# Optimization experiments

Measured on AMD Instinct MI355X. Metric: run time of the kernel, lower is better.

Reference implementation:

```python
import jax, jax.numpy as jnp
import numpy as np

N = 50000
E = 800000
NUM_GRAPHS = 64
D_IN = 261
D_SAGE = 64
D_LIN = 32
N_SAGE_REST = 6
N_LIN_REST = 3
EPS = 1e-5


def _layernorm(x, g, b):
    mu = jnp.mean(x, axis=-1, keepdims=True)
    var = jnp.mean((x - mu) ** 2, axis=-1, keepdims=True)
    return (x - mu) * jax.lax.rsqrt(var + EPS) * g + b


def _sage_block(x, Wl, bl, Wr, g, b, src, dst, inv_deg, residual):
    # mean aggregation of neighbor (source) features onto targets
    msum = jax.ops.segment_sum(x[src], dst, num_segments=N)  # [N, d]
    mean = msum * inv_deg  # [N, d]
    f = mean @ Wl + bl + x @ Wr  # lin_l(aggr) + lin_r(x); lin_r has no bias
    f = jax.nn.gelu(f, approximate=False)
    f = _layernorm(f, g, b)
    if residual:
        f = f + x
    return f


def _lin_block(x, W, b, g, beta, residual):
    f = jax.nn.gelu(x @ W + b, approximate=False)
    f = _layernorm(f, g, beta)
    if residual:
        f = f + x
    return f


def setup_inputs() -> dict:
    key = jax.random.key(0)
    ks = jax.random.split(key, 24)
    x = jax.random.normal(ks[0], (N, D_IN), dtype=jnp.float32)
    edge_index = jax.random.randint(ks[1], (2, E), 0, N, dtype=jnp.int64)
    batch = jnp.sort(jax.random.randint(ks[2], (N,), 0, NUM_GRAPHS, dtype=jnp.int64))

    def glorot(k, shape):
        fan_in = shape[0]
        return jax.random.normal(k, shape, dtype=jnp.float32) / np.sqrt(fan_in)

    inp = {
        "x": x, "edge_index": edge_index, "batch": batch,
        # first SAGE block (261 -> 64, no residual)
        "Wl0": glorot(ks[3], (D_IN, D_SAGE)), "bl0": jnp.zeros((D_SAGE,), jnp.float32),
        "Wr0": glorot(ks[4], (D_IN, D_SAGE)),
        "g0": jnp.ones((D_SAGE,), jnp.float32), "beta0": jnp.zeros((D_SAGE,), jnp.float32),
        # 6 residual SAGE blocks (64 -> 64), stacked
        "Wl": glorot(ks[5], (N_SAGE_REST, D_SAGE, D_SAGE)),
        "bl": jnp.zeros((N_SAGE_REST, D_SAGE), jnp.float32),
        "Wr": glorot(ks[6], (N_SAGE_REST, D_SAGE, D_SAGE)),
        "g": jnp.ones((N_SAGE_REST, D_SAGE), jnp.float32),
        "beta": jnp.zeros((N_SAGE_REST, D_SAGE), jnp.float32),
        # MLP: first LinearBlock 64 -> 32 (no residual)
        "M0": glorot(ks[7], (D_SAGE, D_LIN)), "mb0": jnp.zeros((D_LIN,), jnp.float32),
        "mg0": jnp.ones((D_LIN,), jnp.float32), "mbeta0": jnp.zeros((D_LIN,), jnp.float32),
        # 3 residual LinearBlocks 32 -> 32, stacked
        "M": glorot(ks[8], (N_LIN_REST, D_LIN, D_LIN)),
        "mb": jnp.zeros((N_LIN_REST, D_LIN), jnp.float32),
        "mg": jnp.ones((N_LIN_REST, D_LIN), jnp.float32),
        "mbeta": jnp.zeros((N_LIN_REST, D_LIN), jnp.float32),
        # final Linear 32 -> 1
        "Wf": glorot(ks[9], (D_LIN, 1)), "bf": jnp.zeros((1,), jnp.float32),
    }
    return inp


def reference(x, edge_index, batch, Wl0, bl0, Wr0, g0, beta0, Wl, bl, Wr, g, beta,
              M0, mb0, mg0, mbeta0, M, mb, mg, mbeta, Wf, bf):
    src, dst = edge_index[0], edge_index[1]
    deg = jax.ops.segment_sum(jnp.ones((E,), x.dtype), dst, num_segments=N)
    inv_deg = (1.0 / jnp.maximum(deg, 1.0))[:, None]  # [N,1]

    h = _sage_block(x, Wl0, bl0, Wr0, g0, beta0, src, dst, inv_deg, residual=False)
    for i in range(N_SAGE_REST):
        h = _sage_block(h, Wl[i], bl[i], Wr[i], g[i], beta[i], src, dst, inv_deg, residual=True)

    pooled = jax.ops.segment_sum(h, batch, num_segments=NUM_GRAPHS)  # [G, 64]

    m = _lin_block(pooled, M0, mb0, mg0, mbeta0, residual=False)
    for i in range(N_LIN_REST):
        m = _lin_block(m, M[i], mb[i], mg[i], mbeta[i], residual=True)
    return m @ Wf + bf  # [G, 1]
```

## Files before the change

### kernel.cpp

```cpp
#include <hip/hip_runtime.h>
#include <hip/hip_bf16.h>
#include <math.h>

#define N_NODES 50000
#define N_EDGES 800000
#define NUM_GRAPHS 64
#define NPAD 50048
#define KPAD0 288
#define PSPLIT 16
#define MAXDEG 64

#define GEMM0_GRID (NPAD / 64)
#define SCAT_GRID  ((N_EDGES + 255) / 256)
#define ZERO_GRID  ((N_NODES + 255) / 256)
#define PREPW_TOT  (128 * KPAD0 + 6 * 128 * 64)
#define PREPW_GRID ((PREPW_TOT + 255) / 256)

typedef __attribute__((ext_vector_type(8))) short short8;
typedef __attribute__((ext_vector_type(4))) float f32x4;

__device__ __forceinline__ float gelu_f(float v) {
    return 0.5f * v * (1.0f + erff(v * 0.70710678118654752440f));
}

__device__ __forceinline__ float half_sum32(float v) {
    v += __shfl_xor(v, 1); v += __shfl_xor(v, 2); v += __shfl_xor(v, 4);
    v += __shfl_xor(v, 8); v += __shfl_xor(v, 16);
    return v;
}

__device__ __forceinline__ float group_sum8(float v) {
    v += __shfl_xor(v, 1); v += __shfl_xor(v, 2); v += __shfl_xor(v, 4);
    return v;
}

__device__ __forceinline__ unsigned short f2bf(float f) {
    unsigned int u = __float_as_uint(f);
    unsigned int r = (u + 0x7fffu + ((u >> 16) & 1u)) >> 16;
    return (unsigned short)r;
}

__device__ __forceinline__ float bf_lo(unsigned int u) {
    return __uint_as_float(u << 16);
}
__device__ __forceinline__ float bf_hi(unsigned int u) {
    return __uint_as_float(u & 0xffff0000u);
}


__global__ void k_prep(int* __restrict__ deg,
                       const float* __restrict__ Wl0, const float* __restrict__ Wr0,
                       const float* __restrict__ Wl, const float* __restrict__ Wr,
                       unsigned short* __restrict__ Bt0, unsigned short* __restrict__ BtR) {
    const int blk = blockIdx.x, tid = threadIdx.x;
    if (blk < ZERO_GRID) {
        int i = blk * 256 + tid;
        if (i < N_NODES) deg[i] = 0;
        return;
    }
    int idx = (blk - ZERO_GRID) * 256 + tid;
    const int n0 = 128 * KPAD0;
    if (idx < n0) {
        int j = idx / KPAD0, k = idx - j * KPAD0;
        float v = 0.0f;
        if (k < 261) v = (j < 64) ? Wl0[k * 64 + j] : Wr0[k * 64 + (j - 64)];
        Bt0[idx] = f2bf(v);
    } else if (idx < PREPW_TOT) {
        int r = idx - n0;
        int l = r >> 13;
        int rr = r & 8191;
        int j = rr >> 6, k = rr & 63;
        float v = (j < 64) ? Wl[l * 4096 + k * 64 + j] : Wr[l * 4096 + k * 64 + (j - 64)];
        BtR[r] = f2bf(v);
    }
}


__global__ __launch_bounds__(256) void k_front(
        const float* __restrict__ X, const unsigned short* __restrict__ Bt0,
        unsigned short* __restrict__ U, float* __restrict__ V,
        const int* __restrict__ src, const int* __restrict__ dst,
        int* __restrict__ deg, unsigned short* __restrict__ col64) {
    __shared__ __align__(16) unsigned short sA[64 * 32];
    __shared__ __align__(16) unsigned short sB[128 * 32];
    const int blk = blockIdx.x;
    const int tid = threadIdx.x;

    if (blk < GEMM0_GRID) {
        const int lane = tid & 63, wid = tid >> 6;
        const int l16 = lane & 15, quad = lane >> 4;
        const int m0 = blk * 64;
        f32x4 acc[8];
        #pragma unroll
        for (int j = 0; j < 8; ++j) { acc[j][0] = 0.f; acc[j][1] = 0.f; acc[j][2] = 0.f; acc[j][3] = 0.f; }
        const int arow = tid >> 2, apart = (tid & 3) << 3;
        const int node = m0 + arow;
        const int rowok = (node < N_NODES);
        for (int kc = 0; kc < KPAD0; kc += 32) {
            if (kc) __syncthreads();
            short8 av;
            #pragma unroll
            for (int j = 0; j < 8; ++j) {
                int kk = kc + apart + j;
                float val = (rowok && kk < 261) ? X[(size_t)node * 261 + kk] : 0.0f;
                av[j] = (short)f2bf(val);
            }
            *(short8*)&sA[arow * 32 + apart] = av;
            #pragma unroll
            for (int q = 0; q < 2; ++q) {
                int flat = q * 256 + tid;
                int br = flat >> 2, bp = (flat & 3) << 3;
                *(int4*)&sB[br * 32 + bp] = *(const int4*)&Bt0[(size_t)br * KPAD0 + kc + bp];
            }
            __syncthreads();
            short8 af = *(const short8*)&sA[(wid * 16 + l16) * 32 + quad * 8];
            #pragma unroll
            for (int j = 0; j < 8; ++j) {
                short8 bf = *(const short8*)&sB[(j * 16 + l16) * 32 + quad * 8];
                acc[j] = __builtin_amdgcn_mfma_f32_16x16x32_bf16(af, bf, acc[j], 0, 0, 0);
            }
        }
        const int rbase = m0 + wid * 16 + quad * 4;
        #pragma unroll
        for (int j = 0; j < 4; ++j)
            #pragma unroll
            for (int r = 0; r < 4; ++r)
                U[(size_t)(rbase + r) * 64 + j * 16 + l16] = f2bf(acc[j][r]);
        #pragma unroll
        for (int j = 4; j < 8; ++j)
            #pragma unroll
            for (int r = 0; r < 4; ++r)
                V[(size_t)(rbase + r) * 64 + (j - 4) * 16 + l16] = acc[j][r];
    } else {
        int i = (blk - GEMM0_GRID) * 256 + tid;
        if (i < N_EDGES) {
            int d = dst[i];
            int pos = atomicAdd(&deg[d], 1);
            if (pos < MAXDEG) col64[(d << 6) + pos] = (unsigned short)src[i];
        }
    }
}


__global__ __launch_bounds__(256) void k_layer(
        const unsigned short* __restrict__ U_in, const float* __restrict__ V_in,
        unsigned short* __restrict__ h,
        float* __restrict__ hf_out,
        const int* __restrict__ deg, const unsigned short* __restrict__ col64,
        const float* __restrict__ bias, const float* __restrict__ gam,
        const float* __restrict__ bet,
        const unsigned short* __restrict__ Bt_next,
        unsigned short* __restrict__ U_out, float* __restrict__ V_out,
        int residual, int have_gemm) {
    __shared__ __align__(16) unsigned short sA[2 * 64 * 32];
    __shared__ __align__(16) unsigned short sB[128 * 32];
    const int tid = threadIdx.x;
    const int lane = tid & 63, wid = tid >> 6;
    const int sub = lane >> 3, hl = lane & 7;
    const int base = lane & 56;
    const int m0 = blockIdx.x * 64;
    const uint4* __restrict__ Up = (const uint4*)U_in;

    #pragma unroll
    for (int rep = 0; rep < 2; ++rep) {
        const int nl = rep * 32 + wid * 8 + sub;
        const int node = m0 + nl;
        const bool valid = (node < N_NODES);
        const int nd = valid ? node : 0;
        const int dg = valid ? deg[nd] : 0;
        const int cnt = min(dg, MAXDEG);
        uint4 cv = make_uint4(0u, 0u, 0u, 0u);
        if (valid) cv = *(const uint4*)&col64[((size_t)nd << 6) + hl * 8];
        float s0 = 0.f, s1 = 0.f, s2 = 0.f, s3 = 0.f, s4 = 0.f, s5 = 0.f, s6 = 0.f, s7 = 0.f;
        for (int b = 0; b * 8 < cnt; b += 2) {
            #pragma unroll
            for (int hh = 0; hh < 2; ++hh) {
                const int sl = base + b + hh;
                unsigned int p0 = (unsigned int)__shfl((int)cv.x, sl);
                unsigned int p1 = (unsigned int)__shfl((int)cv.y, sl);
                unsigned int p2 = (unsigned int)__shfl((int)cv.z, sl);
                unsigned int p3 = (unsigned int)__shfl((int)cv.w, sl);
                const int eb = (b + hh) * 8;
                int c[8];
                c[0] = (int)(p0 & 0xffffu); c[1] = (int)(p0 >> 16);
                c[2] = (int)(p1 & 0xffffu); c[3] = (int)(p1 >> 16);
                c[4] = (int)(p2 & 0xffffu); c[5] = (int)(p2 >> 16);
                c[6] = (int)(p3 & 0xffffu); c[7] = (int)(p3 >> 16);
                #pragma unroll
                for (int i = 0; i < 8; ++i) {
                    uint4 u = (eb + i < cnt) ? Up[(size_t)c[i] * 8 + hl] : make_uint4(0u, 0u, 0u, 0u);
                    s0 += bf_lo(u.x); s1 += bf_hi(u.x);
                    s2 += bf_lo(u.y); s3 += bf_hi(u.y);
                    s4 += bf_lo(u.z); s5 += bf_hi(u.z);
                    s6 += bf_lo(u.w); s7 += bf_hi(u.w);
                }
            }
        }
        const float id = 1.0f / fmaxf((float)dg, 1.0f);
        const float4 b0 = *(const float4*)&bias[8 * hl];
        const float4 b1 = *(const float4*)&bias[8 * hl + 4];
        float4 v0 = make_float4(0.f, 0.f, 0.f, 0.f), v1 = v0;
        if (valid) {
            v0 = *(const float4*)&V_in[(size_t)nd * 64 + 8 * hl];
            v1 = *(const float4*)&V_in[(size_t)nd * 64 + 8 * hl + 4];
        }
        float f0 = gelu_f(s0 * id + b0.x + v0.x);
        float f1 = gelu_f(s1 * id + b0.y + v0.y);
        float f2 = gelu_f(s2 * id + b0.z + v0.z);
        float f3 = gelu_f(s3 * id + b0.w + v0.w);
        float f4 = gelu_f(s4 * id + b1.x + v1.x);
        float f5 = gelu_f(s5 * id + b1.y + v1.y);
        float f6 = gelu_f(s6 * id + b1.z + v1.z);
        float f7 = gelu_f(s7 * id + b1.w + v1.w);
        float mu = group_sum8(((f0 + f1) + (f2 + f3)) + ((f4 + f5) + (f6 + f7))) * 0.015625f;
        float d0 = f0 - mu, d1 = f1 - mu, d2 = f2 - mu, d3 = f3 - mu;
        float d4 = f4 - mu, d5 = f5 - mu, d6 = f6 - mu, d7 = f7 - mu;
        float var = group_sum8(((d0 * d0 + d1 * d1) + (d2 * d2 + d3 * d3)) +
                               ((d4 * d4 + d5 * d5) + (d6 * d6 + d7 * d7))) * 0.015625f;
        float rs = rsqrtf(var + 1e-5f);
        const float4 g0v = *(const float4*)&gam[8 * hl];
        const float4 g1v = *(const float4*)&gam[8 * hl + 4];
        const float4 e0v = *(const float4*)&bet[8 * hl];
        const float4 e1v = *(const float4*)&bet[8 * hl + 4];
        f0 = d0 * rs * g0v.x + e0v.x;
        f1 = d1 * rs * g0v.y + e0v.y;
        f2 = d2 * rs * g0v.z + e0v.z;
        f3 = d3 * rs * g0v.w + e0v.w;
        f4 = d4 * rs * g1v.x + e1v.x;
        f5 = d5 * rs * g1v.y + e1v.y;
        f6 = d6 * rs * g1v.z + e1v.z;
        f7 = d7 * rs * g1v.w + e1v.w;
        if (residual && valid) {
            uint4 hu = ((const uint4*)h)[(size_t)nd * 8 + hl];
            f0 += bf_lo(hu.x); f1 += bf_hi(hu.x);
            f2 += bf_lo(hu.y); f3 += bf_hi(hu.y);
            f4 += bf_lo(hu.z); f5 += bf_hi(hu.z);
            f6 += bf_lo(hu.w); f7 += bf_hi(hu.w);
        }
        uint4 outw;
        outw.x = (unsigned int)f2bf(f0) | ((unsigned int)f2bf(f1) << 16);
        outw.y = (unsigned int)f2bf(f2) | ((unsigned int)f2bf(f3) << 16);
        outw.z = (unsigned int)f2bf(f4) | ((unsigned int)f2bf(f5) << 16);
        outw.w = (unsigned int)f2bf(f6) | ((unsigned int)f2bf(f7) << 16);
        if (valid) {
            ((uint4*)h)[(size_t)nd * 8 + hl] = outw;
            if (hf_out) {
                *(float4*)&hf_out[(size_t)nd * 64 + 8 * hl] = make_float4(f0, f1, f2, f3);
                *(float4*)&hf_out[(size_t)nd * 64 + 8 * hl + 4] = make_float4(f4, f5, f6, f7);
            }
        }
        *(uint4*)&sA[(((hl >> 2) * 64 + nl) << 5) + (hl & 3) * 8] = outw;
    }
    if (!have_gemm) return;
    __syncthreads();

    const int l16 = lane & 15, quad = lane >> 4;
    f32x4 acc[8];
    #pragma unroll
    for (int j = 0; j < 8; ++j) { acc[j][0] = 0.f; acc[j][1] = 0.f; acc[j][2] = 0.f; acc[j][3] = 0.f; }
    for (int kc = 0; kc < 64; kc += 32) {
        if (kc) __syncthreads();
        #pragma unroll
        for (int q = 0; q < 2; ++q) {
            int flat = q * 256 + tid;
            int br = flat >> 2, bp = (flat & 3) << 3;
            *(int4*)&sB[br * 32 + bp] = *(const int4*)&Bt_next[(size_t)br * 64 + kc + bp];
        }
        __syncthreads();
        short8 af = *(const short8*)&sA[(((kc >> 5) * 64 + wid * 16 + l16) << 5) + quad * 8];
        #pragma unroll
        for (int j = 0; j < 8; ++j) {
            short8 bf = *(const short8*)&sB[(j * 16 + l16) * 32 + quad * 8];
            acc[j] = __builtin_amdgcn_mfma_f32_16x16x32_bf16(af, bf, acc[j], 0, 0, 0);
        }
    }
    const int rbase = m0 + wid * 16 + quad * 4;
    #pragma unroll
    for (int j = 0; j < 4; ++j)
        #pragma unroll
        for (int r = 0; r < 4; ++r)
            U_out[(size_t)(rbase + r) * 64 + j * 16 + l16] = f2bf(acc[j][r]);
    #pragma unroll
    for (int j = 4; j < 8; ++j)
        #pragma unroll
        for (int r = 0; r < 4; ++r)
            V_out[(size_t)(rbase + r) * 64 + (j - 4) * 16 + l16] = acc[j][r];
}


__global__ __launch_bounds__(256) void k_pool1(const float* __restrict__ h, const int* __restrict__ batch,
                                               float* __restrict__ partial, int n) {
    __shared__ float sred[4][64];
    const int g = blockIdx.x / PSPLIT;
    const int s = blockIdx.x - g * PSPLIT;
    const int lane = threadIdx.x & 63, wid = threadIdx.x >> 6;
    int lo = 0, hi = n;
    while (lo < hi) { int mid = (lo + hi) >> 1; if (batch[mid] < g) lo = mid + 1; else hi = mid; }
    const int start = lo;
    lo = 0; hi = n;
    while (lo < hi) { int mid = (lo + hi) >> 1; if (batch[mid] < g + 1) lo = mid + 1; else hi = mid; }
    const int end = lo;
    const int len = end - start;
    const int chunk = (len + PSPLIT - 1) / PSPLIT;
    const int a = start + s * chunk;
    const int b = min(a + chunk, end);
    float sum = 0.0f;
    for (int node = a + wid; node < b; node += 4) sum += h[(size_t)node * 64 + lane];
    sred[wid][lane] = sum;
    __syncthreads();
    if (wid == 0)
        partial[(size_t)blockIdx.x * 64 + lane] = sred[0][lane] + sred[1][lane] + sred[2][lane] + sred[3][lane];
}


__global__ __launch_bounds__(1024) void k_head(const float* __restrict__ partial,
                                               const float* __restrict__ M0, const float* __restrict__ mb0,
                                               const float* __restrict__ mg0, const float* __restrict__ mbeta0,
                                               const float* __restrict__ M, const float* __restrict__ mb,
                                               const float* __restrict__ mg, const float* __restrict__ mbeta,
                                               const float* __restrict__ Wf, const float* __restrict__ bf,
                                               float* __restrict__ out) {
    __shared__ float sP[64 * 64];
    __shared__ float sA[64 * 33];
    __shared__ float sB[64 * 33];
    const int tx = threadIdx.x, ty = threadIdx.y;
    const int tid = ty * 32 + tx;
    for (int i = tid; i < 64 * 64; i += 1024) {
        int g = i >> 6, f = i & 63;
        float s = 0.0f;
        #pragma unroll
        for (int s2 = 0; s2 < PSPLIT; ++s2) s += partial[(size_t)(g * PSPLIT + s2) * 64 + f];
        sP[i] = s;
    }
    __syncthreads();
    #pragma unroll
    for (int rr = 0; rr < 2; ++rr) {
        int r = ty + rr * 32;
        float a = mb0[tx];
        for (int k = 0; k < 64; ++k) a += sP[r * 64 + k] * M0[k * 32 + tx];
        a = gelu_f(a);
        float mu = half_sum32(a) * (1.0f / 32.0f);
        float d = a - mu;
        float var = half_sum32(d * d) * (1.0f / 32.0f);
        a = d * rsqrtf(var + 1e-5f) * mg0[tx] + mbeta0[tx];
        sA[r * 33 + tx] = a;
    }
    __syncthreads();
    float* cur = sA;
    float* nxt = sB;
    for (int L = 0; L < 3; ++L) {
        const float* Mi = M + L * 32 * 32;
        const float* mbi = mb + L * 32;
        const float* mgi = mg + L * 32;
        const float* mbetai = mbeta + L * 32;
        #pragma unroll
        for (int rr = 0; rr < 2; ++rr) {
            int r = ty + rr * 32;
            float a = mbi[tx];
            for (int k = 0; k < 32; ++k) a += cur[r * 33 + k] * Mi[k * 32 + tx];
            a = gelu_f(a);
            float mu = half_sum32(a) * (1.0f / 32.0f);
            float d = a - mu;
            float var = half_sum32(d * d) * (1.0f / 32.0f);
            a = d * rsqrtf(var + 1e-5f) * mgi[tx] + mbetai[tx] + cur[r * 33 + tx];
            nxt[r * 33 + tx] = a;
        }
        __syncthreads();
        float* t = cur; cur = nxt; nxt = t;
    }
    #pragma unroll
    for (int rr = 0; rr < 2; ++rr) {
        int r = ty + rr * 32;
        float p = cur[r * 33 + tx] * Wf[tx];
        p = half_sum32(p);
        if (tx == 0) out[r] = p + bf[0];
    }
}


extern "C" void kernel_launch(void* const* d_in, const int* in_sizes, int n_in,
                              void* d_out, int out_size, void* d_ws, size_t ws_size,
                              hipStream_t stream) {
    const int N = N_NODES;
    const int E = N_EDGES;

    const float* x    = (const float*)d_in[0];
    const int* eidx   = (const int*)d_in[1];
    const int* batch  = (const int*)d_in[2];
    const float* Wl0  = (const float*)d_in[3];
    const float* bl0  = (const float*)d_in[4];
    const float* Wr0  = (const float*)d_in[5];
    const float* g0   = (const float*)d_in[6];
    const float* bet0 = (const float*)d_in[7];
    const float* Wl   = (const float*)d_in[8];
    const float* bl   = (const float*)d_in[9];
    const float* Wr   = (const float*)d_in[10];
    const float* gR   = (const float*)d_in[11];
    const float* betR = (const float*)d_in[12];
    const float* M0   = (const float*)d_in[13];
    const float* mb0  = (const float*)d_in[14];
    const float* mg0  = (const float*)d_in[15];
    const float* mbe0 = (const float*)d_in[16];
    const float* M    = (const float*)d_in[17];
    const float* mb   = (const float*)d_in[18];
    const float* mg   = (const float*)d_in[19];
    const float* mbe  = (const float*)d_in[20];
    const float* Wf   = (const float*)d_in[21];
    const float* bf   = (const float*)d_in[22];

    const int* src = eidx;
    const int* dst = eidx + E;

    char* p = (char*)d_ws;
    auto alloc = [&](size_t bytes) -> void* {
        void* q = (void*)p;
        p += (bytes + 255) & ~(size_t)255;
        return q;
    };
    int*   deg    = (int*)alloc((size_t)N * 4);
    unsigned short* col64 = (unsigned short*)alloc((size_t)N * MAXDEG * 2);
    unsigned short* Bt0 = (unsigned short*)alloc((size_t)128 * KPAD0 * 2);
    unsigned short* BtR = (unsigned short*)alloc((size_t)6 * 128 * 64 * 2);
    unsigned short* Ua  = (unsigned short*)alloc((size_t)NPAD * 64 * 2);
    unsigned short* Ub  = (unsigned short*)alloc((size_t)NPAD * 64 * 2);
    float* Va   = (float*)alloc((size_t)NPAD * 64 * 4);
    float* Vb   = (float*)alloc((size_t)NPAD * 64 * 4);
    unsigned short* hbuf = (unsigned short*)alloc((size_t)NPAD * 64 * 2);
    float* partial = (float*)alloc((size_t)NUM_GRAPHS * PSPLIT * 64 * 4);

    k_prep<<<ZERO_GRID + PREPW_GRID, 256, 0, stream>>>(deg, Wl0, Wr0, Wl, Wr, Bt0, BtR);

    k_front<<<GEMM0_GRID + SCAT_GRID, 256, 0, stream>>>(
        x, Bt0, Ua, Va, src, dst, deg, col64);

    unsigned short* Uin = Ua;  float* Vin = Va;
    unsigned short* Uout = Ub; float* Vout = Vb;
    for (int i = 0; i < 7; ++i) {
        const float* bias = (i == 0) ? bl0  : bl  + (size_t)(i - 1) * 64;
        const float* gam  = (i == 0) ? g0   : gR  + (size_t)(i - 1) * 64;
        const float* bet  = (i == 0) ? bet0 : betR + (size_t)(i - 1) * 64;
        const int have_gemm = (i < 6);
        float* hf = (i == 6) ? Vout : nullptr;
        k_layer<<<GEMM0_GRID, 256, 0, stream>>>(
            Uin, Vin, hbuf, hf, deg, col64, bias, gam, bet,
            have_gemm ? (BtR + (size_t)i * 128 * 64) : BtR,
            Uout, Vout, (i > 0) ? 1 : 0, have_gemm);
        unsigned short* tu = Uin; Uin = Uout; Uout = tu;
        float* tv = Vin; Vin = Vout; Vout = tv;
    }
    float* hf_final = Vin;

    k_pool1<<<NUM_GRAPHS * PSPLIT, 256, 0, stream>>>(hf_final, batch, partial, N);
    k_head<<<1, dim3(32, 32), 0, stream>>>(partial, M0, mb0, mg0, mbe0, M, mb, mg, mbe, Wf, bf, (float*)d_out);
}
```

Baseline: 409.6 us.

## Split front kernel, slice edge scatter by destination range, halve layer tile

Separates the fused GEMM0/edge-scatter kernel into two launches. The scatter now runs with each block scanning a chunk of edges 8 times, once per destination slice, so atomics into deg/col64 stay inside a narrower address range for locality. k_layer now handles 32 nodes per block instead of 64, doubling the grid. Its GEMM is split across waves by row half and output half, and launch bounds request higher occupancy. The tradeoffs are 8x reads of src/dst, an extra launch, and a smaller MFMA tile per block.

```diff
diff --git a/kernel.cpp b/kernel.cpp
--- a/kernel.cpp
+++ b/kernel.cpp
@@ -11,10 +11,16 @@
 #define MAXDEG 64
 
 #define GEMM0_GRID (NPAD / 64)
-#define SCAT_GRID  ((N_EDGES + 255) / 256)
+#define LAYER_GRID (NPAD / 32)
 #define ZERO_GRID  ((N_NODES + 255) / 256)
 #define PREPW_TOT  (128 * KPAD0 + 6 * 128 * 64)
 #define PREPW_GRID ((PREPW_TOT + 255) / 256)
+
+#define SLICES 8
+#define NPS 6250
+#define SCHUNK 2048
+#define SCHUNKS ((N_EDGES + SCHUNK - 1) / SCHUNK)
+#define SCAT_GRID (SCHUNKS * SLICES)
 
 typedef __attribute__((ext_vector_type(8))) short short8;
 typedef __attribute__((ext_vector_type(4))) float f32x4;
@@ -76,73 +82,78 @@
 }
 
 
-__global__ __launch_bounds__(256) void k_front(
+__global__ __launch_bounds__(256) void k_gemm0(
         const float* __restrict__ X, const unsigned short* __restrict__ Bt0,
-        unsigned short* __restrict__ U, float* __restrict__ V,
+        unsigned short* __restrict__ U, float* __restrict__ V) {
+    __shared__ __align__(16) unsigned short sA[64 * 32];
+    __shared__ __align__(16) unsigned short sB[128 * 32];
+    const int tid = threadIdx.x;
+    const int lane = tid & 63, wid = tid >> 6;
+    const int l16 = lane & 15, quad = lane >> 4;
+    const int m0 = blockIdx.x * 64;
+    f32x4 acc[8];
+    #pragma unroll
+    for (int j = 0; j < 8; ++j) { acc[j][0] = 0.f; acc[j][1] = 0.f; acc[j][2] = 0.f; acc[j][3] = 0.f; }
+    const int arow = tid >> 2, apart = (tid & 3) << 3;
+    const int node = m0 + arow;
+    const int rowok = (node < N_NODES);
+    for (int kc = 0; kc < KPAD0; kc += 32) {
+        if (kc) __syncthreads();
+        short8 av;
+        #pragma unroll
+        for (int j = 0; j < 8; ++j) {
+            int kk = kc + apart + j;
+            float val = (rowok && kk < 261) ? X[(size_t)node * 261 + kk] : 0.0f;
+            av[j] = (short)f2bf(val);
+        }
+        *(short8*)&sA[arow * 32 + apart] = av;
+        #pragma unroll
+        for (int q = 0; q < 2; ++q) {
+            int flat = q * 256 + tid;
+            int br = flat >> 2, bp = (flat & 3) << 3;
+            *(int4*)&sB[br * 32 + bp] = *(const int4*)&Bt0[(size_t)br * KPAD0 + kc + bp];
+        }
+        __syncthreads();
+        short8 af = *(const short8*)&sA[(wid * 16 + l16) * 32 + quad * 8];
+        #pragma unroll
+        for (int j = 0; j < 8; ++j) {
+            short8 bf = *(const short8*)&sB[(j * 16 + l16) * 32 + quad * 8];
+            acc[j] = __builtin_amdgcn_mfma_f32_16x16x32_bf16(af, bf, acc[j], 0, 0, 0);
+        }
+    }
+    const int rbase = m0 + wid * 16 + quad * 4;
+    #pragma unroll
+    for (int j = 0; j < 4; ++j)
+        #pragma unroll
+        for (int r = 0; r < 4; ++r)
+            U[(size_t)(rbase + r) * 64 + j * 16 + l16] = f2bf(acc[j][r]);
+    #pragma unroll
+    for (int j = 4; j < 8; ++j)
+        #pragma unroll
+        for (int r = 0; r < 4; ++r)
+            V[(size_t)(rbase + r) * 64 + (j - 4) * 16 + l16] = acc[j][r];
+}
+
+
+__global__ __launch_bounds__(256) void k_scat(
         const int* __restrict__ src, const int* __restrict__ dst,
         int* __restrict__ deg, unsigned short* __restrict__ col64) {
-    __shared__ __align__(16) unsigned short sA[64 * 32];
-    __shared__ __align__(16) unsigned short sB[128 * 32];
-    const int blk = blockIdx.x;
-    const int tid = threadIdx.x;
-
-    if (blk < GEMM0_GRID) {
-        const int lane = tid & 63, wid = tid >> 6;
-        const int l16 = lane & 15, quad = lane >> 4;
-        const int m0 = blk * 64;
-        f32x4 acc[8];
-        #pragma unroll
-        for (int j = 0; j < 8; ++j) { acc[j][0] = 0.f; acc[j][1] = 0.f; acc[j][2] = 0.f; acc[j][3] = 0.f; }
-        const int arow = tid >> 2, apart = (tid & 3) << 3;
-        const int node = m0 + arow;
-        const int rowok = (node < N_NODES);
-        for (int kc = 0; kc < KPAD0; kc += 32) {
-            if (kc) __syncthreads();
-            short8 av;
-            #pragma unroll
-            for (int j = 0; j < 8; ++j) {
-                int kk = kc + apart + j;
-                float val = (rowok && kk < 261) ? X[(size_t)node * 261 + kk] : 0.0f;
-                av[j] = (short)f2bf(val);
-            }
-            *(short8*)&sA[arow * 32 + apart] = av;
-            #pragma unroll
-            for (int q = 0; q < 2; ++q) {
-                int flat = q * 256 + tid;
-                int br = flat >> 2, bp = (flat & 3) << 3;
-                *(int4*)&sB[br * 32 + bp] = *(const int4*)&Bt0[(size_t)br * KPAD0 + kc + bp];
-            }
-            __syncthreads();
-            short8 af = *(const short8*)&sA[(wid * 16 + l16) * 32 + quad * 8];
-            #pragma unroll
-            for (int j = 0; j < 8; ++j) {
-                short8 bf = *(const short8*)&sB[(j * 16 + l16) * 32 + quad * 8];
-                acc[j] = __builtin_amdgcn_mfma_f32_16x16x32_bf16(af, bf, acc[j], 0, 0, 0);
-            }
-        }
-        const int rbase = m0 + wid * 16 + quad * 4;
-        #pragma unroll
-        for (int j = 0; j < 4; ++j)
-            #pragma unroll
-            for (int r = 0; r < 4; ++r)
-                U[(size_t)(rbase + r) * 64 + j * 16 + l16] = f2bf(acc[j][r]);
-        #pragma unroll
-        for (int j = 4; j < 8; ++j)
-            #pragma unroll
-            for (int r = 0; r < 4; ++r)
-                V[(size_t)(rbase + r) * 64 + (j - 4) * 16 + l16] = acc[j][r];
-    } else {
-        int i = (blk - GEMM0_GRID) * 256 + tid;
-        if (i < N_EDGES) {
-            int d = dst[i];
+    const int s = blockIdx.x & (SLICES - 1);
+    const int c = blockIdx.x >> 3;
+    const int base = c * SCHUNK;
+    const int lim = min(base + SCHUNK, N_EDGES);
+    for (int i = base + (int)threadIdx.x; i < lim; i += 256) {
+        int d = dst[i];
+        int sv = src[i];
+        if (d / NPS == s) {
             int pos = atomicAdd(&deg[d], 1);
-            if (pos < MAXDEG) col64[(d << 6) + pos] = (unsigned short)src[i];
-        }
-    }
-}
-
-
-__global__ __launch_bounds__(256) void k_layer(
+            if (pos < MAXDEG) col64[(d << 6) + pos] = (unsigned short)sv;
+        }
+    }
+}
+
+
+__global__ __launch_bounds__(256, 4) void k_layer(
         const unsigned short* __restrict__ U_in, const float* __restrict__ V_in,
         unsigned short* __restrict__ h,
         float* __restrict__ hf_out,
@@ -152,112 +163,111 @@
         const unsigned short* __restrict__ Bt_next,
         unsigned short* __restrict__ U_out, float* __restrict__ V_out,
         int residual, int have_gemm) {
-    __shared__ __align__(16) unsigned short sA[2 * 64 * 32];
+    __shared__ __align__(16) unsigned short sA[2 * 32 * 32];
     __shared__ __align__(16) unsigned short sB[128 * 32];
     const int tid = threadIdx.x;
     const int lane = tid & 63, wid = tid >> 6;
     const int sub = lane >> 3, hl = lane & 7;
     const int base = lane & 56;
-    const int m0 = blockIdx.x * 64;
+    const int m0 = blockIdx.x * 32;
     const uint4* __restrict__ Up = (const uint4*)U_in;
 
-    #pragma unroll
-    for (int rep = 0; rep < 2; ++rep) {
-        const int nl = rep * 32 + wid * 8 + sub;
-        const int node = m0 + nl;
-        const bool valid = (node < N_NODES);
-        const int nd = valid ? node : 0;
-        const int dg = valid ? deg[nd] : 0;
-        const int cnt = min(dg, MAXDEG);
-        uint4 cv = make_uint4(0u, 0u, 0u, 0u);
-        if (valid) cv = *(const uint4*)&col64[((size_t)nd << 6) + hl * 8];
-        float s0 = 0.f, s1 = 0.f, s2 = 0.f, s3 = 0.f, s4 = 0.f, s5 = 0.f, s6 = 0.f, s7 = 0.f;
-        for (int b = 0; b * 8 < cnt; b += 2) {
+    const int nl = wid * 8 + sub;
+    const int node = m0 + nl;
+    const bool valid = (node < N_NODES);
+    const int nd = valid ? node : 0;
+    const int dg = valid ? deg[nd] : 0;
+    const int cnt = min(dg, MAXDEG);
+    uint4 cv = make_uint4(0u, 0u, 0u, 0u);
+    if (valid) cv = *(const uint4*)&col64[((size_t)nd << 6) + hl * 8];
+    float s0 = 0.f, s1 = 0.f, s2 = 0.f, s3 = 0.f, s4 = 0.f, s5 = 0.f, s6 = 0.f, s7 = 0.f;
+    for (int b = 0; b * 8 < cnt; b += 2) {
+        #pragma unroll
+        for (int hh = 0; hh < 2; ++hh) {
+            const int sl = base + b + hh;
+            unsigned int p0 = (unsigned int)__shfl((int)cv.x, sl);
+            unsigned int p1 = (unsigned int)__shfl((int)cv.y, sl);
+            unsigned int p2 = (unsigned int)__shfl((int)cv.z, sl);
+            unsigned int p3 = (unsigned int)__shfl((int)cv.w, sl);
+            const int eb = (b + hh) * 8;
+            int c[8];
+            c[0] = (int)(p0 & 0xffffu); c[1] = (int)(p0 >> 16);
+            c[2] = (int)(p1 & 0xffffu); c[3] = (int)(p1 >> 16);
+            c[4] = (int)(p2 & 0xffffu); c[5] = (int)(p2 >> 16);
+            c[6] = (int)(p3 & 0xffffu); c[7] = (int)(p3 >> 16);
             #pragma unroll
-            for (int hh = 0; hh < 2; ++hh) {
-                const int sl = base + b + hh;
-                unsigned int p0 = (unsigned int)__shfl((int)cv.x, sl);
-                unsigned int p1 = (unsigned int)__shfl((int)cv.y, sl);
-                unsigned int p2 = (unsigned int)__shfl((int)cv.z, sl);
-                unsigned int p3 = (unsigned int)__shfl((int)cv.w, sl);
-                const int eb = (b + hh) * 8;
-                int c[8];
-                c[0] = (int)(p0 & 0xffffu); c[1] = (int)(p0 >> 16);
-                c[2] = (int)(p1 & 0xffffu); c[3] = (int)(p1 >> 16);
-                c[4] = (int)(p2 & 0xffffu); c[5] = (int)(p2 >> 16);
-                c[6] = (int)(p3 & 0xffffu); c[7] = (int)(p3 >> 16);
-                #pragma unroll
-                for (int i = 0; i < 8; ++i) {
-                    uint4 u = (eb + i < cnt) ? Up[(size_t)c[i] * 8 + hl] : make_uint4(0u, 0u, 0u, 0u);
-                    s0 += bf_lo(u.x); s1 += bf_hi(u.x);
-                    s2 += bf_lo(u.y); s3 += bf_hi(u.y);
-                    s4 += bf_lo(u.z); s5 += bf_hi(u.z);
-                    s6 += bf_lo(u.w); s7 += bf_hi(u.w);
-                }
+            for (int i = 0; i < 8; ++i) {
+                uint4 u = (eb + i < cnt) ? Up[(size_t)c[i] * 8 + hl] : make_uint4(0u, 0u, 0u, 0u);
+                s0 += bf_lo(u.x); s1 += bf_hi(u.x);
+                s2 += bf_lo(u.y); s3 += bf_hi(u.y);
+                s4 += bf_lo(u.z); s5 += bf_hi(u.z);
+                s6 += bf_lo(u.w); s7 += bf_hi(u.w);
             }
         }
-        const float id = 1.0f / fmaxf((float)dg, 1.0f);
-        const float4 b0 = *(const float4*)&bias[8 * hl];
-        const float4 b1 = *(const float4*)&bias[8 * hl + 4];
-        float4 v0 = make_float4(0.f, 0.f, 0.f, 0.f), v1 = v0;
-        if (valid) {
-            v0 = *(const float4*)&V_in[(size_t)nd * 64 + 8 * hl];
-            v1 = *(const float4*)&V_in[(size_t)nd * 64 + 8 * hl + 4];
-        }
-        float f0 = gelu_f(s0 * id + b0.x + v0.x);
-        float f1 = gelu_f(s1 * id + b0.y + v0.y);
-        float f2 = gelu_f(s2 * id + b0.z + v0.z);
-        float f3 = gelu_f(s3 * id + b0.w + v0.w);
-        float f4 = gelu_f(s4 * id + b1.x + v1.x);
-        float f5 = gelu_f(s5 * id + b1.y + v1.y);
-        float f6 = gelu_f(s6 * id + b1.z + v1.z);
-        float f7 = gelu_f(s7 * id + b1.w + v1.w);
-        float mu = group_sum8(((f0 + f1) + (f2 + f3)) + ((f4 + f5) + (f6 + f7))) * 0.015625f;
-        float d0 = f0 - mu, d1 = f1 - mu, d2 = f2 - mu, d3 = f3 - mu;
-        float d4 = f4 - mu, d5 = f5 - mu, d6 = f6 - mu, d7 = f7 - mu;
-        float var = group_sum8(((d0 * d0 + d1 * d1) + (d2 * d2 + d3 * d3)) +
-                               ((d4 * d4 + d5 * d5) + (d6 * d6 + d7 * d7))) * 0.015625f;
-        float rs = rsqrtf(var + 1e-5f);
-        const float4 g0v = *(const float4*)&gam[8 * hl];
-        const float4 g1v = *(const float4*)&gam[8 * hl + 4];
-        const float4 e0v = *(const float4*)&bet[8 * hl];
-        const float4 e1v = *(const float4*)&bet[8 * hl + 4];
-        f0 = d0 * rs * g0v.x + e0v.x;
-        f1 = d1 * rs * g0v.y + e0v.y;
-        f2 = d2 * rs * g0v.z + e0v.z;
-        f3 = d3 * rs * g0v.w + e0v.w;
-        f4 = d4 * rs * g1v.x + e1v.x;
-        f5 = d5 * rs * g1v.y + e1v.y;
-        f6 = d6 * rs * g1v.z + e1v.z;
-        f7 = d7 * rs * g1v.w + e1v.w;
-        if (residual && valid) {
-            uint4 hu = ((const uint4*)h)[(size_t)nd * 8 + hl];
-            f0 += bf_lo(hu.x); f1 += bf_hi(hu.x);
-            f2 += bf_lo(hu.y); f3 += bf_hi(hu.y);
-            f4 += bf_lo(hu.z); f5 += bf_hi(hu.z);
-            f6 += bf_lo(hu.w); f7 += bf_hi(hu.w);
-        }
-        uint4 outw;
-        outw.x = (unsigned int)f2bf(f0) | ((unsigned int)f2bf(f1) << 16);
-        outw.y = (unsigned int)f2bf(f2) | ((unsigned int)f2bf(f3) << 16);
-        outw.z = (unsigned int)f2bf(f4) | ((unsigned int)f2bf(f5) << 16);
-        outw.w = (unsigned int)f2bf(f6) | ((unsigned int)f2bf(f7) << 16);
-        if (valid) {
-            ((uint4*)h)[(size_t)nd * 8 + hl] = outw;
-            if (hf_out) {
-                *(float4*)&hf_out[(size_t)nd * 64 + 8 * hl] = make_float4(f0, f1, f2, f3);
-                *(float4*)&hf_out[(size_t)nd * 64 + 8 * hl + 4] = make_float4(f4, f5, f6, f7);
-            }
-        }
-        *(uint4*)&sA[(((hl >> 2) * 64 + nl) << 5) + (hl & 3) * 8] = outw;
-    }
+    }
+    const float id = 1.0f / fmaxf((float)dg, 1.0f);
+    const float4 b0 = *(const float4*)&bias[8 * hl];
+    const float4 b1 = *(const float4*)&bias[8 * hl + 4];
+    float4 v0 = make_float4(0.f, 0.f, 0.f, 0.f), v1 = v0;
+    if (valid) {
+        v0 = *(const float4*)&V_in[(size_t)nd * 64 + 8 * hl];
+        v1 = *(const float4*)&V_in[(size_t)nd * 64 + 8 * hl + 4];
+    }
+    float f0 = gelu_f(s0 * id + b0.x + v0.x);
+    float f1 = gelu_f(s1 * id + b0.y + v0.y);
+    float f2 = gelu_f(s2 * id + b0.z + v0.z);
+    float f3 = gelu_f(s3 * id + b0.w + v0.w);
+    float f4 = gelu_f(s4 * id + b1.x + v1.x);
+    float f5 = gelu_f(s5 * id + b1.y + v1.y);
+    float f6 = gelu_f(s6 * id + b1.z + v1.z);
+    float f7 = gelu_f(s7 * id + b1.w + v1.w);
+    float mu = group_sum8(((f0 + f1) + (f2 + f3)) + ((f4 + f5) + (f6 + f7))) * 0.015625f;
+    float d0 = f0 - mu, d1 = f1 - mu, d2 = f2 - mu, d3 = f3 - mu;
+    float d4 = f4 - mu, d5 = f5 - mu, d6 = f6 - mu, d7 = f7 - mu;
+    float var = group_sum8(((d0 * d0 + d1 * d1) + (d2 * d2 + d3 * d3)) +
+                           ((d4 * d4 + d5 * d5) + (d6 * d6 + d7 * d7))) * 0.015625f;
+    float rs = rsqrtf(var + 1e-5f);
+    const float4 g0v = *(const float4*)&gam[8 * hl];
+    const float4 g1v = *(const float4*)&gam[8 * hl + 4];
+    const float4 e0v = *(const float4*)&bet[8 * hl];
+    const float4 e1v = *(const float4*)&bet[8 * hl + 4];
+    f0 = d0 * rs * g0v.x + e0v.x;
+    f1 = d1 * rs * g0v.y + e0v.y;
+    f2 = d2 * rs * g0v.z + e0v.z;
+    f3 = d3 * rs * g0v.w + e0v.w;
+    f4 = d4 * rs * g1v.x + e1v.x;
+    f5 = d5 * rs * g1v.y + e1v.y;
+    f6 = d6 * rs * g1v.z + e1v.z;
+    f7 = d7 * rs * g1v.w + e1v.w;
+    if (residual && valid) {
+        uint4 hu = ((const uint4*)h)[(size_t)nd * 8 + hl];
+        f0 += bf_lo(hu.x); f1 += bf_hi(hu.x);
+        f2 += bf_lo(hu.y); f3 += bf_hi(hu.y);
+        f4 += bf_lo(hu.z); f5 += bf_hi(hu.z);
+        f6 += bf_lo(hu.w); f7 += bf_hi(hu.w);
+    }
+    uint4 outw;
+    outw.x = (unsigned int)f2bf(f0) | ((unsigned int)f2bf(f1) << 16);
+    outw.y = (unsigned int)f2bf(f2) | ((unsigned int)f2bf(f3) << 16);
+    outw.z = (unsigned int)f2bf(f4) | ((unsigned int)f2bf(f5) << 16);
+    outw.w = (unsigned int)f2bf(f6) | ((unsigned int)f2bf(f7) << 16);
+    if (valid) {
+        ((uint4*)h)[(size_t)nd * 8 + hl] = outw;
+        if (hf_out) {
+            *(float4*)&hf_out[(size_t)nd * 64 + 8 * hl] = make_float4(f0, f1, f2, f3);
+            *(float4*)&hf_out[(size_t)nd * 64 + 8 * hl + 4] = make_float4(f4, f5, f6, f7);
+        }
+    }
+    *(uint4*)&sA[(((hl >> 2) * 32 + nl) << 5) + (hl & 3) * 8] = outw;
+
     if (!have_gemm) return;
     __syncthreads();
 
     const int l16 = lane & 15, quad = lane >> 4;
-    f32x4 acc[8];
-    #pragma unroll
-    for (int j = 0; j < 8; ++j) { acc[j][0] = 0.f; acc[j][1] = 0.f; acc[j][2] = 0.f; acc[j][3] = 0.f; }
+    const int wrow = wid & 1, colh = wid >> 1;
+    f32x4 acc[4];
+    #pragma unroll
+    for (int j = 0; j < 4; ++j) { acc[j][0] = 0.f; acc[j][1] = 0.f; acc[j][2] = 0.f; acc[j][3] = 0.f; }
     for (int kc = 0; kc < 64; kc += 32) {
         if (kc) __syncthreads();
         #pragma unroll
@@ -267,24 +277,27 @@
             *(int4*)&sB[br * 32 + bp] = *(const int4*)&Bt_next[(size_t)br * 64 + kc + bp];
         }
         __syncthreads();
-        short8 af = *(const short8*)&sA[(((kc >> 5) * 64 + wid * 16 + l16) << 5) + quad * 8];
-        #pragma unroll
-        for (int j = 0; j < 8; ++j) {
-            short8 bf = *(const short8*)&sB[(j * 16 + l16) * 32 + quad * 8];
+        short8 af = *(const short8*)&sA[(((kc >> 5) * 32 + wrow * 16 + l16) << 5) + quad * 8];
+        #pragma unroll
+        for (int j = 0; j < 4; ++j) {
+            short8 bf = *(const short8*)&sB[(colh * 64 + j * 16 + l16) * 32 + quad * 8];
             acc[j] = __builtin_amdgcn_mfma_f32_16x16x32_bf16(af, bf, acc[j], 0, 0, 0);
         }
     }
-    const int rbase = m0 + wid * 16 + quad * 4;
-    #pragma unroll
-    for (int j = 0; j < 4; ++j)
-        #pragma unroll
-        for (int r = 0; r < 4; ++r)
-            U_out[(size_t)(rbase + r) * 64 + j * 16 + l16] = f2bf(acc[j][r]);
-    #pragma unroll
-    for (int j = 4; j < 8; ++j)
-        #pragma unroll
-        for (int r = 0; r < 4; ++r)
-            V_out[(size_t)(rbase + r) * 64 + (j - 4) * 16 + l16] = acc[j][r];
+    const int rbase = m0 + wrow * 16 + quad * 4;
+    if (colh == 0) {
+        #pragma unroll
+        for (int j = 0; j < 4; ++j)
+            #pragma unroll
+            for (int r = 0; r < 4; ++r)
+                U_out[(size_t)(rbase + r) * 64 + j * 16 + l16] = f2bf(acc[j][r]);
+    } else {
+        #pragma unroll
+        for (int j = 0; j < 4; ++j)
+            #pragma unroll
+            for (int r = 0; r < 4; ++r)
+                V_out[(size_t)(rbase + r) * 64 + j * 16 + l16] = acc[j][r];
+    }
 }
 
 
@@ -430,8 +443,9 @@
 
     k_prep<<<ZERO_GRID + PREPW_GRID, 256, 0, stream>>>(deg, Wl0, Wr0, Wl, Wr, Bt0, BtR);
 
-    k_front<<<GEMM0_GRID + SCAT_GRID, 256, 0, stream>>>(
-        x, Bt0, Ua, Va, src, dst, deg, col64);
+    k_scat<<<SCAT_GRID, 256, 0, stream>>>(src, dst, deg, col64);
+
+    k_gemm0<<<GEMM0_GRID, 256, 0, stream>>>(x, Bt0, Ua, Va);
 
     unsigned short* Uin = Ua;  float* Vin = Va;
     unsigned short* Uout = Ub; float* Vout = Vb;
@@ -441,7 +455,7 @@
         const float* bet  = (i == 0) ? bet0 : betR + (size_t)(i - 1) * 64;
         const int have_gemm = (i < 6);
         float* hf = (i == 6) ? Vout : nullptr;
-        k_layer<<<GEMM0_GRID, 256, 0, stream>>>(
+        k_layer<<<LAYER_GRID, 256, 0, stream>>>(
             Uin, Vin, hbuf, hf, deg, col64, bias, gam, bet,
             have_gemm ? (BtR + (size_t)i * 128 * 64) : BtR,
             Uout, Vout, (i > 0) ? 1 : 0, have_gemm);
```

Measured after the change: 375.4 us. -8.3%, faster.
